# Performance work log

Measured on AMD Instinct MI355X. Metric: run time of the kernel, lower is better.

The kernel has to match this reference:

```python
import jax, jax.numpy as jnp
import numpy as np

D_MODEL = 1024
N_HEAD = 16
HEAD_DIM = D_MODEL // N_HEAD
D_FF = 4096
N_EXPERTS = 4
EPS = 1e-05


def _layer_norm(x, gamma, beta):
    mu = jnp.mean(x, axis=-1, keepdims=True)
    var = jnp.mean((x - mu) ** 2, axis=-1, keepdims=True)
    return (x - mu) / jnp.sqrt(var + EPS) * gamma + beta


def setup_inputs() -> dict:
    key = jax.random.key(0)
    ks = jax.random.split(key, 20)
    f32 = jnp.float32
    sc = 1.0 / np.sqrt(D_MODEL)
    scf = 1.0 / np.sqrt(D_FF)
    return {
        "src": jax.random.normal(ks[0], (4, 512, D_MODEL), f32),
        "Wq": jax.random.normal(ks[1], (D_MODEL, D_MODEL), f32) * sc,
        "bq": jnp.zeros((D_MODEL,), f32),
        "Wk": jax.random.normal(ks[2], (D_MODEL, D_MODEL), f32) * sc,
        "bk": jnp.zeros((D_MODEL,), f32),
        "Wv": jax.random.normal(ks[3], (D_MODEL, D_MODEL), f32) * sc,
        "bv": jnp.zeros((D_MODEL,), f32),
        "Wo": jax.random.normal(ks[4], (D_MODEL, D_MODEL), f32) * sc,
        "bo": jnp.zeros((D_MODEL,), f32),
        "router_w": jax.random.normal(ks[5], (D_MODEL, 1), f32) * 0.05,
        "router_b": jnp.zeros((1,), f32),
        "W1": jax.random.normal(ks[6], (N_EXPERTS, D_MODEL, D_FF), f32) * sc,
        "b1": jnp.zeros((N_EXPERTS, D_FF), f32),
        "W2": jax.random.normal(ks[7], (N_EXPERTS, D_FF, D_MODEL), f32) * scf,
        "b2": jnp.zeros((N_EXPERTS, D_MODEL), f32),
        "ln1_g": jnp.ones((D_MODEL,), f32),
        "ln1_b": jnp.zeros((D_MODEL,), f32),
        "ln2_g": jnp.ones((D_MODEL,), f32),
        "ln2_b": jnp.zeros((D_MODEL,), f32),
    }


def reference(src, Wq, bq, Wk, bk, Wv, bv, Wo, bo, router_w, router_b,
              W1, b1, W2, b2, ln1_g, ln1_b, ln2_g, ln2_b):
    B, T, _ = src.shape
    # --- self attention ---
    q = (src @ Wq + bq).reshape(B, T, N_HEAD, HEAD_DIM)
    k = (src @ Wk + bk).reshape(B, T, N_HEAD, HEAD_DIM)
    v = (src @ Wv + bv).reshape(B, T, N_HEAD, HEAD_DIM)
    scale = HEAD_DIM ** -0.5
    scores = jnp.einsum('bqhd,bkhd->bhqk', q, k) * scale
    probs = jax.nn.softmax(scores, axis=-1)
    attn = jnp.einsum('bhqk,bkhd->bqhd', probs, v).reshape(B, T, D_MODEL)
    attn = attn @ Wo + bo
    x = _layer_norm(src + attn, ln1_g, ln1_b)
    # --- hash-routed single-expert MoE FFN ---
    keys = (x @ router_w + router_b)[..., 0]           # [B, T]
    expert_idx = jnp.remainder(jnp.floor(keys).astype(jnp.int32), N_EXPERTS)
    ff_out = jnp.zeros_like(x)
    for e in range(N_EXPERTS):
        h = jax.nn.relu(x @ W1[e] + b1[e])             # [B, T, D_FF]
        y = h @ W2[e] + b2[e]                          # [B, T, D_MODEL]
        ff_out = ff_out + jnp.where((expert_idx == e)[..., None], y, 0.0)
    return _layer_norm(x + ff_out, ln2_g, ln2_b)
```

## Files before the change

### kernel.cpp

```cpp
#include <hip/hip_runtime.h>
#include <hip/hip_bf16.h>
#include <stdint.h>

typedef unsigned short u16;
typedef __attribute__((ext_vector_type(8))) short s8v;
typedef __attribute__((ext_vector_type(4))) float f4v;

#define DEVI static __device__ __forceinline__

DEVI u16 f2bf(float x) {
  union { float f; unsigned u; } a; a.f = x;
  return (u16)((a.u + 0x7fffu + ((a.u >> 16) & 1u)) >> 16);
}
DEVI float bf2f(u16 h) {
  union { float f; unsigned u; } a; a.u = ((unsigned)h) << 16; return a.f;
}
DEVI float wred_add(float s) {
#pragma unroll
  for (int o = 32; o; o >>= 1) s += __shfl_xor(s, o, 64);
  return s;
}
DEVI float wred_max(float s) {
#pragma unroll
  for (int o = 32; o; o >>= 1) s = fmaxf(s, __shfl_xor(s, o, 64));
  return s;
}
DEVI f4v mfma16(s8v a, s8v b, f4v c) {
  return __builtin_amdgcn_mfma_f32_16x16x32_bf16(a, b, c, 0, 0, 0);
}

DEVI void gload16(const u16* gp, u16* lp) {
  __builtin_amdgcn_global_load_lds(
      (const __attribute__((address_space(1))) uint32_t*)gp,
      (__attribute__((address_space(3))) uint32_t*)lp, 16, 0, 0);
}

DEVI s8v ldfrag_sw(const u16* base, int r, int lg) {
  const u16* row = base + r * 32;
  const int x = (r >> 1) & 3;
  const int hl = (lg & 1) * 4;
  const int g1 = lg >> 1;
  union { s8v v; uint2 u[2]; } t;
  t.u[0] = *(const uint2*)(row + ((g1 ^ x) * 8) + hl);
  t.u[1] = *(const uint2*)(row + (((g1 + 2) ^ x) * 8) + hl);
  return t.v;
}

__global__ __launch_bounds__(256) void split_k(const float* __restrict__ in,
                                               u16* __restrict__ h, u16* __restrict__ l, int n4) {
  int i = blockIdx.x * 256 + threadIdx.x;
  if (i >= n4) return;
  float4 v = ((const float4*)in)[i];
  ushort4 hv, lv;
  hv.x = f2bf(v.x); lv.x = f2bf(v.x - bf2f(hv.x));
  hv.y = f2bf(v.y); lv.y = f2bf(v.y - bf2f(hv.y));
  hv.z = f2bf(v.z); lv.z = f2bf(v.z - bf2f(hv.z));
  hv.w = f2bf(v.w); lv.w = f2bf(v.w - bf2f(hv.w));
  ((ushort4*)h)[i] = hv;
  ((ushort4*)l)[i] = lv;
}

template<bool LO>
__global__ __launch_bounds__(256) void transpose_split_k(const float* __restrict__ in, long long zIn,
                                                         u16* __restrict__ outH, u16* __restrict__ outL,
                                                         long long zOut, int R, int C) {
  __shared__ float t[32][33];
  in += (long long)blockIdx.z * zIn;
  outH += (long long)blockIdx.z * zOut;
  if (LO) outL += (long long)blockIdx.z * zOut;
  const int cc = blockIdx.x * 32, rr = blockIdx.y * 32;
  const int tx = threadIdx.x, ty = threadIdx.y;
#pragma unroll
  for (int i = 0; i < 4; ++i)
    t[ty * 4 + i][tx] = in[(long long)(rr + ty * 4 + i) * C + cc + tx];
  __syncthreads();
#pragma unroll
  for (int i = 0; i < 4; ++i) {
    float v = t[tx][ty * 4 + i];
    long long o = (long long)(cc + ty * 4 + i) * R + rr + tx;
    u16 h = f2bf(v);
    outH[o] = h;
    if (LO) outL[o] = f2bf(v - bf2f(h));
  }
}

__global__ __launch_bounds__(256) void transpose_pair_k(const u16* __restrict__ inH, const u16* __restrict__ inL,
                                                        u16* __restrict__ oH, u16* __restrict__ oL) {
  __shared__ u16 th[32][34], tl[32][34];
  const int b = blockIdx.z;
  const int dd = blockIdx.x * 32;
  const int tt = blockIdx.y * 32;
  const int tx = threadIdx.x, ty = threadIdx.y;
  const int64_t ibase = ((int64_t)(b * 512 + tt)) * 3072 + 2048 + dd;
#pragma unroll
  for (int i = 0; i < 4; ++i) {
    int rr = ty * 4 + i;
    th[rr][tx] = inH[ibase + (int64_t)rr * 3072 + tx];
    tl[rr][tx] = inL[ibase + (int64_t)rr * 3072 + tx];
  }
  __syncthreads();
  const int64_t obase = ((int64_t)b * 1024 + dd) * 512 + tt;
#pragma unroll
  for (int i = 0; i < 4; ++i) {
    int rr = ty * 4 + i;
    oH[obase + (int64_t)rr * 512 + tx] = th[tx][rr];
    oL[obase + (int64_t)rr * 512 + tx] = tl[tx][rr];
  }
}

__global__ __launch_bounds__(256) void catb_k(const float* __restrict__ a, const float* __restrict__ b,
                                              const float* __restrict__ c, float* __restrict__ o) {
  int i = blockIdx.x * 256 + threadIdx.x;
  if (i >= 3072) return;
  o[i] = i < 1024 ? a[i] : (i < 2048 ? b[i - 1024] : c[i - 2048]);
}

struct GemmArgs {
  const u16* Ah; const u16* Al; int lda;
  const u16* Bh; const u16* Bl; int ldb;
  float* C; u16* Ch; u16* Cl; int ldc;
  const float* bias;
  int K;
  int Z2;
  int64_t aZ1, aZ2, bZ1, bZ2, cZ1, cZ2;
  const int* ofs;
  int64_t bStrE; int biasStrE;
};

template<int BM, int BN, bool SPLIT, int EPI>
__global__ __launch_bounds__(256) void gemm_k(GemmArgs g) {
  constexpr int ASZ = BM * 32, BSZ = BN * 32;
  constexpr int AN = SPLIT ? 2 * ASZ : ASZ;
  constexpr int BNT = SPLIT ? 2 * BSZ : BSZ;
  __shared__ __align__(16) u16 sA[2][AN];
  __shared__ __align__(16) u16 sB[2][BNT];

  const int tid = threadIdx.x;
  const u16* Ah = g.Ah; const u16* Al = g.Al;
  const u16* Bh = g.Bh; const u16* Bl = g.Bl;
  int64_t cOff = 0;
  if (g.Z2 > 0) {
    int z1 = blockIdx.z / g.Z2, z2 = blockIdx.z % g.Z2;
    int64_t ao = (int64_t)z1 * g.aZ1 + (int64_t)z2 * g.aZ2;
    int64_t bo = (int64_t)z1 * g.bZ1 + (int64_t)z2 * g.bZ2;
    Ah += ao; Bh += bo;
    if (SPLIT) { Al += ao; Bl += bo; }
    cOff = (int64_t)z1 * g.cZ1 + (int64_t)z2 * g.cZ2;
  }
  const int row0 = blockIdx.x * BM;
  const int col0 = blockIdx.y * BN;
  const float* bias = g.bias;
  if (g.ofs) {
    if (row0 >= g.ofs[4]) return;
    int e = 0;
    while (e < 3 && row0 >= g.ofs[e + 1]) ++e;
    Bh += (int64_t)e * g.bStrE;
    if (bias) bias += (int64_t)e * g.biasStrE;
  }

  const int w = tid >> 6, lane = tid & 63;
  const int wr = w >> 1, wc = w & 1;
  const int lr = lane & 15, lg = lane >> 4;
  constexpr int FM = BM / 32, FN = BN / 32;

  const int srow = lane >> 2;
  const int sG = (lane & 3) ^ ((lane >> 3) & 3);

  auto stage = [&](int b, int kt) {
#pragma unroll
    for (int c = 0; c < BM / 64; ++c) {
      int ch = c * 4 + w;
      int64_t go = (int64_t)(row0 + ch * 16 + srow) * g.lda + kt + sG * 8;
      gload16(Ah + go, &sA[b][ch * 512]);
      if (SPLIT) gload16(Al + go, &sA[b][ASZ + ch * 512]);
    }
#pragma unroll
    for (int c = 0; c < BN / 64; ++c) {
      int ch = c * 4 + w;
      int64_t go = (int64_t)(col0 + ch * 16 + srow) * g.ldb + kt + sG * 8;
      gload16(Bh + go, &sB[b][ch * 512]);
      if (SPLIT) gload16(Bl + go, &sB[b][BSZ + ch * 512]);
    }
  };

  f4v acc[FM][FN];
#pragma unroll
  for (int i = 0; i < FM; ++i)
#pragma unroll
    for (int j = 0; j < FN; ++j) acc[i][j] = f4v{0.f, 0.f, 0.f, 0.f};

  stage(0, 0);
  __syncthreads();
  const int nt = g.K >> 5;
  for (int t = 0; t < nt; ++t) {
    const int cur = t & 1;
    if (t + 1 < nt) stage(cur ^ 1, (t + 1) << 5);
    s8v af[FM], bfr[FN], afl[SPLIT ? FM : 1], bfl[SPLIT ? FN : 1];
#pragma unroll
    for (int mi = 0; mi < FM; ++mi) {
      int r = wr * (BM / 2) + mi * 16 + lr;
      af[mi] = ldfrag_sw(&sA[cur][0], r, lg);
      if (SPLIT) afl[mi] = ldfrag_sw(&sA[cur][ASZ], r, lg);
    }
#pragma unroll
    for (int ni = 0; ni < FN; ++ni) {
      int r = wc * (BN / 2) + ni * 16 + lr;
      bfr[ni] = ldfrag_sw(&sB[cur][0], r, lg);
      if (SPLIT) bfl[ni] = ldfrag_sw(&sB[cur][BSZ], r, lg);
    }
#pragma unroll
    for (int mi = 0; mi < FM; ++mi)
#pragma unroll
      for (int ni = 0; ni < FN; ++ni) {
        acc[mi][ni] = mfma16(af[mi], bfr[ni], acc[mi][ni]);
        if (SPLIT) {
          acc[mi][ni] = mfma16(af[mi], bfl[ni], acc[mi][ni]);
          acc[mi][ni] = mfma16(afl[mi], bfr[ni], acc[mi][ni]);
        }
      }
    __syncthreads();
  }
#pragma unroll
  for (int mi = 0; mi < FM; ++mi) {
    int rbase = row0 + wr * (BM / 2) + mi * 16 + lg * 4;
#pragma unroll
    for (int ni = 0; ni < FN; ++ni) {
      int c = col0 + wc * (BN / 2) + ni * 16 + lr;
      float bv = bias ? bias[c] : 0.f;
#pragma unroll
      for (int j = 0; j < 4; ++j) {
        int r = rbase + j;
        float v = acc[mi][ni][j] + bv;
        if (EPI == 0) {
          g.C[cOff + (int64_t)r * g.ldc + c] = v;
        } else if (EPI == 1) {
          u16 h = f2bf(v);
          int64_t o = cOff + (int64_t)r * g.ldc + c;
          g.Ch[o] = h;
          g.Cl[o] = f2bf(v - bf2f(h));
        } else {
          v = v > 0.f ? v : 0.f;
          g.Ch[cOff + (int64_t)r * g.ldc + c] = f2bf(v);
        }
      }
    }
  }
}

__global__ __launch_bounds__(256) void reduce_k(const float* __restrict__ part, const int* __restrict__ rowsrc,
                                                const int* __restrict__ ofs, const float* __restrict__ b2,
                                                float* __restrict__ y) {
  int r = blockIdx.x;
  if (r >= ofs[4]) return;
  int s = rowsrc[r];
  if (s < 0) return;
  int e = 0;
  while (e < 3 && r >= ofs[e + 1]) ++e;
  int c = threadIdx.x;
  const int64_t RN = 2560ll * 1024;
  float4 v0 = ((const float4*)(part + 0 * RN + (int64_t)r * 1024))[c];
  float4 v1 = ((const float4*)(part + 1 * RN + (int64_t)r * 1024))[c];
  float4 v2 = ((const float4*)(part + 2 * RN + (int64_t)r * 1024))[c];
  float4 v3 = ((const float4*)(part + 3 * RN + (int64_t)r * 1024))[c];
  float4 bb = ((const float4*)(b2 + (int64_t)e * 1024))[c];
  float4 o;
  o.x = ((v0.x + v1.x) + v2.x) + v3.x + bb.x;
  o.y = ((v0.y + v1.y) + v2.y) + v3.y + bb.y;
  o.z = ((v0.z + v1.z) + v2.z) + v3.z + bb.z;
  o.w = ((v0.w + v1.w) + v2.w) + v3.w + bb.w;
  ((float4*)(y + (int64_t)s * 1024))[c] = o;
}

__global__ __launch_bounds__(128) void softmax_k(float* __restrict__ scores) {
  __shared__ float sm[2];
  const int64_t row = blockIdx.x;
  float* p = scores + row * 512;
  const int tid = threadIdx.x, w = tid >> 6, lane = tid & 63;
  float4 v = ((const float4*)p)[tid];
  v.x *= 0.125f; v.y *= 0.125f; v.z *= 0.125f; v.w *= 0.125f;
  float m = wred_max(fmaxf(fmaxf(v.x, v.y), fmaxf(v.z, v.w)));
  if (lane == 0) sm[w] = m;
  __syncthreads();
  m = fmaxf(sm[0], sm[1]);
  float e0 = expf(v.x - m), e1 = expf(v.y - m), e2 = expf(v.z - m), e3 = expf(v.w - m);
  float s = wred_add(e0 + e1 + e2 + e3);
  __syncthreads();
  if (lane == 0) sm[w] = s;
  __syncthreads();
  float inv = 1.f / (sm[0] + sm[1]);
  e0 *= inv; e1 *= inv; e2 *= inv; e3 *= inv;
  u16* ph = (u16*)p;
  ushort4 hv, lv;
  hv.x = f2bf(e0); lv.x = f2bf(e0 - bf2f(hv.x));
  hv.y = f2bf(e1); lv.y = f2bf(e1 - bf2f(hv.y));
  hv.z = f2bf(e2); lv.z = f2bf(e2 - bf2f(hv.z));
  hv.w = f2bf(e3); lv.w = f2bf(e3 - bf2f(hv.w));
  ((ushort4*)ph)[tid] = hv;
  ((ushort4*)(ph + 512))[tid] = lv;
}

__global__ __launch_bounds__(256) void ln_k(const float* __restrict__ a, const float* __restrict__ b,
                                            const float* __restrict__ gm, const float* __restrict__ bt,
                                            float* __restrict__ out) {
  __shared__ float sm[4];
  const int r = blockIdx.x, tid = threadIdx.x;
  const int w = tid >> 6, lane = tid & 63;
  float4 va = ((const float4*)(a + (int64_t)r * 1024))[tid];
  float4 vb = ((const float4*)(b + (int64_t)r * 1024))[tid];
  float x0 = va.x + vb.x, x1 = va.y + vb.y, x2 = va.z + vb.z, x3 = va.w + vb.w;
  float s = wred_add(x0 + x1 + x2 + x3);
  if (lane == 0) sm[w] = s;
  __syncthreads();
  float mu = (sm[0] + sm[1] + sm[2] + sm[3]) * (1.f / 1024.f);
  float d0 = x0 - mu, d1 = x1 - mu, d2 = x2 - mu, d3 = x3 - mu;
  float q = wred_add(d0 * d0 + d1 * d1 + d2 * d2 + d3 * d3);
  __syncthreads();
  if (lane == 0) sm[w] = q;
  __syncthreads();
  float var = (sm[0] + sm[1] + sm[2] + sm[3]) * (1.f / 1024.f);
  float rs = 1.f / sqrtf(var + 1e-5f);
  float4 g4 = ((const float4*)gm)[tid];
  float4 b4 = ((const float4*)bt)[tid];
  float4 o;
  o.x = d0 * rs * g4.x + b4.x;
  o.y = d1 * rs * g4.y + b4.y;
  o.z = d2 * rs * g4.z + b4.z;
  o.w = d3 * rs * g4.w + b4.w;
  ((float4*)(out + (int64_t)r * 1024))[tid] = o;
}

__global__ __launch_bounds__(256) void router_k(const float* __restrict__ x, const float* __restrict__ rw,
                                                const float* __restrict__ rb, int* __restrict__ eidx) {
  int t = blockIdx.x * 4 + (threadIdx.x >> 6);
  int lane = threadIdx.x & 63;
  const float* xr = x + (int64_t)t * 1024;
  float s = 0.f;
#pragma unroll
  for (int i = 0; i < 16; ++i) {
    int c = i * 64 + lane;
    s += xr[c] * rw[c];
  }
  s = wred_add(s);
  if (lane == 0) {
    float key = s + rb[0];
    int f = (int)floorf(key);
    eidx[t] = f & 3;
  }
}

__global__ __launch_bounds__(256) void compact_k(const int* __restrict__ eidx,
                                                 int* __restrict__ rowsrc, int* __restrict__ ofs) {
  __shared__ unsigned long long sc[256];
  __shared__ int soff[5];
  const int tid = threadIdx.x;
  int myE[8];
  unsigned long long c = 0;
#pragma unroll
  for (int i = 0; i < 8; ++i) {
    int e = eidx[tid * 8 + i];
    myE[i] = e;
    c += 1ull << (e * 16);
  }
  sc[tid] = c;
  __syncthreads();
  for (int o = 1; o < 256; o <<= 1) {
    unsigned long long v = (tid >= o) ? sc[tid - o] : 0ull;
    __syncthreads();
    sc[tid] += v;
    __syncthreads();
  }
  unsigned long long incl = sc[tid], tot = sc[255];
  unsigned long long excl = incl - c;
  if (tid == 0) {
    int off = 0;
    for (int e = 0; e < 4; ++e) {
      soff[e] = off;
      int cnt = (int)((tot >> (e * 16)) & 0xffff);
      off += (cnt + 127) & ~127;
    }
    soff[4] = off;
    for (int e = 0; e < 5; ++e) ofs[e] = soff[e];
  }
  __syncthreads();
  for (int r = tid; r < 2560; r += 256) rowsrc[r] = -1;
  __threadfence_block();
  __syncthreads();
  int rank[4];
#pragma unroll
  for (int e = 0; e < 4; ++e) rank[e] = (int)((excl >> (e * 16)) & 0xffff);
#pragma unroll
  for (int i = 0; i < 8; ++i) {
    int e = myE[i];
    rowsrc[soff[e] + rank[e]] = tid * 8 + i;
    rank[e]++;
  }
}

__global__ __launch_bounds__(256) void gather_k(const float* __restrict__ x, const int* __restrict__ rowsrc,
                                                const int* __restrict__ ofs, u16* __restrict__ xg) {
  int r = blockIdx.x;
  if (r >= ofs[4]) return;
  int s = rowsrc[r];
  int c = threadIdx.x;
  float4 v = (s >= 0) ? ((const float4*)(x + (int64_t)s * 1024))[c] : float4{0.f, 0.f, 0.f, 0.f};
  ushort4 o;
  o.x = f2bf(v.x); o.y = f2bf(v.y); o.z = f2bf(v.z); o.w = f2bf(v.w);
  ((ushort4*)(xg + (int64_t)r * 1024))[c] = o;
}

extern "C" void kernel_launch(void* const* d_in, const int* in_sizes, int n_in,
                              void* d_out, int out_size, void* d_ws, size_t ws_size,
                              hipStream_t stream) {
  const float* src = (const float*)d_in[0];
  const float* Wq  = (const float*)d_in[1];
  const float* bq  = (const float*)d_in[2];
  const float* Wk  = (const float*)d_in[3];
  const float* bk  = (const float*)d_in[4];
  const float* Wv  = (const float*)d_in[5];
  const float* bv  = (const float*)d_in[6];
  const float* Wo  = (const float*)d_in[7];
  const float* bo  = (const float*)d_in[8];
  const float* rw  = (const float*)d_in[9];
  const float* rb  = (const float*)d_in[10];
  const float* W1  = (const float*)d_in[11];
  const float* b1  = (const float*)d_in[12];
  const float* W2  = (const float*)d_in[13];
  const float* b2  = (const float*)d_in[14];
  const float* g1  = (const float*)d_in[15];
  const float* be1 = (const float*)d_in[16];
  const float* g2  = (const float*)d_in[17];
  const float* be2 = (const float*)d_in[18];
  float* out = (float*)d_out;

  char* base = (char*)d_ws;
  size_t off = 0;
  auto alloc = [&](size_t bytes) -> char* {
    char* p = base + off;
    off += (bytes + 255) & ~(size_t)255;
    return p;
  };
  const size_t MB = 1ull << 20;
  u16* srcH = (u16*)alloc(4 * MB);
  u16* srcL = (u16*)alloc(4 * MB);
  u16* WqkvTh = (u16*)alloc(6 * MB);
  u16* WqkvTl = (u16*)alloc(6 * MB);
  u16* WoTh = (u16*)alloc(2 * MB);
  u16* WoTl = (u16*)alloc(2 * MB);
  float* bqkv = (float*)alloc(16 * 1024);
  u16* qkvH = (u16*)alloc(12 * MB);
  u16* qkvL = (u16*)alloc(12 * MB);
  u16* hbuf = (u16*)qkvH;
  u16* vTH = (u16*)alloc(4 * MB); u16* vTL = (u16*)alloc(4 * MB);
  float* scores = (float*)alloc(64 * MB);
  u16* W1T = (u16*)scores;
  u16* W2T = (u16*)scores + 16ull * 1024 * 1024;
  u16* attnH = (u16*)alloc(4 * MB); u16* attnL = (u16*)alloc(4 * MB);
  u16* xg = (u16*)attnH;
  float* woOut = (float*)alloc(8 * MB);
  float* ybuf = (float*)woOut;
  float* xbuf = (float*)alloc(8 * MB);
  float* partials = (float*)alloc(40 * MB);
  int* eidx   = (int*)alloc(2048 * 4);
  int* rowsrc = (int*)alloc(2560 * 4);
  int* ofs    = (int*)alloc(32);
  (void)ws_size; (void)in_sizes; (void)n_in; (void)out_size;

  dim3 tb(32, 8);

  split_k<<<2048, 256, 0, stream>>>(src, srcH, srcL, 2048 * 1024 / 4);
  transpose_split_k<true><<<dim3(32, 32, 1), tb, 0, stream>>>(Wq, 0, WqkvTh, WqkvTl, 0, 1024, 1024);
  transpose_split_k<true><<<dim3(32, 32, 1), tb, 0, stream>>>(Wk, 0, WqkvTh + 1024 * 1024, WqkvTl + 1024 * 1024, 0, 1024, 1024);
  transpose_split_k<true><<<dim3(32, 32, 1), tb, 0, stream>>>(Wv, 0, WqkvTh + 2 * 1024 * 1024, WqkvTl + 2 * 1024 * 1024, 0, 1024, 1024);
  transpose_split_k<true><<<dim3(32, 32, 1), tb, 0, stream>>>(Wo, 0, WoTh, WoTl, 0, 1024, 1024);
  catb_k<<<12, 256, 0, stream>>>(bq, bk, bv, bqkv);

  {
    GemmArgs g{};
    g.Ah = srcH; g.Al = srcL; g.lda = 1024;
    g.Bh = WqkvTh; g.Bl = WqkvTl; g.ldb = 1024;
    g.Ch = qkvH; g.Cl = qkvL; g.ldc = 3072;
    g.bias = bqkv; g.K = 1024; g.Z2 = 0;
    gemm_k<128, 64, true, 1><<<dim3(16, 48, 1), 256, 0, stream>>>(g);
  }
  transpose_pair_k<<<dim3(32, 16, 4), tb, 0, stream>>>(qkvH, qkvL, vTH, vTL);

  {
    GemmArgs g{};
    g.Ah = qkvH; g.Al = qkvL; g.lda = 3072;
    g.Bh = qkvH + 1024; g.Bl = qkvL + 1024; g.ldb = 3072;
    g.C = scores; g.ldc = 512;
    g.K = 64; g.Z2 = 16;
    g.aZ1 = 512ll * 3072; g.aZ2 = 64;
    g.bZ1 = 512ll * 3072; g.bZ2 = 64;
    g.cZ1 = 16ll * 512 * 512; g.cZ2 = 512ll * 512;
    gemm_k<128, 64, true, 0><<<dim3(4, 8, 64), 256, 0, stream>>>(g);
  }
  softmax_k<<<64 * 512, 128, 0, stream>>>(scores);
  {
    GemmArgs g{};
    g.Ah = (const u16*)scores; g.Al = (const u16*)scores + 512; g.lda = 1024;
    g.Bh = vTH; g.Bl = vTL; g.ldb = 512;
    g.Ch = attnH; g.Cl = attnL; g.ldc = 1024;
    g.K = 512; g.Z2 = 16;
    g.aZ1 = 16ll * 512 * 1024; g.aZ2 = 512ll * 1024;
    g.bZ1 = 1024ll * 512;      g.bZ2 = 64ll * 512;
    g.cZ1 = 512ll * 1024;      g.cZ2 = 64;
    gemm_k<64, 64, true, 1><<<dim3(8, 1, 64), 256, 0, stream>>>(g);
  }
  {
    GemmArgs g{};
    g.Ah = attnH; g.Al = attnL; g.lda = 1024;
    g.Bh = WoTh; g.Bl = WoTl; g.ldb = 1024;
    g.C = woOut; g.ldc = 1024;
    g.bias = bo; g.K = 1024; g.Z2 = 0;
    gemm_k<64, 64, true, 0><<<dim3(32, 16, 1), 256, 0, stream>>>(g);
  }
  ln_k<<<2048, 256, 0, stream>>>(src, woOut, g1, be1, xbuf);

  router_k<<<512, 256, 0, stream>>>(xbuf, rw, rb, eidx);
  compact_k<<<1, 256, 0, stream>>>(eidx, rowsrc, ofs);
  gather_k<<<2560, 256, 0, stream>>>(xbuf, rowsrc, ofs, xg);

  transpose_split_k<false><<<dim3(128, 32, 4), tb, 0, stream>>>(W1, 1024ll * 4096, W1T, nullptr, 4096ll * 1024, 1024, 4096);
  transpose_split_k<false><<<dim3(32, 128, 4), tb, 0, stream>>>(W2, 4096ll * 1024, W2T, nullptr, 1024ll * 4096, 4096, 1024);

  {
    GemmArgs g{};
    g.Ah = xg; g.lda = 1024;
    g.Bh = W1T; g.ldb = 1024;
    g.Ch = hbuf; g.ldc = 4096;
    g.bias = b1; g.biasStrE = 4096;
    g.K = 1024; g.Z2 = 0;
    g.ofs = ofs; g.bStrE = 4096ll * 1024;
    gemm_k<128, 128, false, 2><<<dim3(20, 32, 1), 256, 0, stream>>>(g);
  }
  {
    GemmArgs g{};
    g.Ah = hbuf; g.lda = 4096;
    g.Bh = W2T; g.ldb = 4096;
    g.C = partials; g.ldc = 1024;
    g.bias = nullptr;
    g.K = 1024; g.Z2 = 4;
    g.aZ1 = 0; g.aZ2 = 1024;
    g.bZ1 = 0; g.bZ2 = 1024;
    g.cZ1 = 0; g.cZ2 = 2560ll * 1024;
    g.ofs = ofs; g.bStrE = 4096ll * 1024;
    gemm_k<128, 64, false, 0><<<dim3(20, 16, 4), 256, 0, stream>>>(g);
  }
  reduce_k<<<2560, 256, 0, stream>>>(partials, rowsrc, ofs, b2, ybuf);
  ln_k<<<2048, 256, 0, stream>>>(xbuf, ybuf, g2, be2, out);
}
```

Before: 335.8 us.

## Permute K within 32-blocks for single 128-bit LDS fragment reads and deepen prefetch

Producers of GEMM operands (split, transpose, gather, GEMM epilogues) now write the K dimension in a permuted order within each 32-element block. Each MFMA fragment can then be read from LDS with one 16-byte load instead of two 8-byte loads. The GEMM main loop also changes from single-buffer-ahead staging to issuing loads two tiles ahead, with explicit vmcnt/lgkmcnt waits and raw barriers. This cuts LDS instruction count and hides more global latency, but it couples the data layout across many kernels and risks subtle correctness errors if any producer and consumer disagree.

```diff
diff --git a/kernel.cpp b/kernel.cpp
--- a/kernel.cpp
+++ b/kernel.cpp
@@ -28,6 +28,8 @@
 DEVI f4v mfma16(s8v a, s8v b, f4v c) {
   return __builtin_amdgcn_mfma_f32_16x16x32_bf16(a, b, c, 0, 0, 0);
 }
+
+DEVI int rho(int j) { return ((j & 12) << 1) | (j & 3) | ((j >> 4) << 2); }
 
 DEVI void gload16(const u16* gp, u16* lp) {
   __builtin_amdgcn_global_load_lds(
@@ -36,14 +38,8 @@
 }
 
 DEVI s8v ldfrag_sw(const u16* base, int r, int lg) {
-  const u16* row = base + r * 32;
-  const int x = (r >> 1) & 3;
-  const int hl = (lg & 1) * 4;
-  const int g1 = lg >> 1;
-  union { s8v v; uint2 u[2]; } t;
-  t.u[0] = *(const uint2*)(row + ((g1 ^ x) * 8) + hl);
-  t.u[1] = *(const uint2*)(row + (((g1 + 2) ^ x) * 8) + hl);
-  return t.v;
+  int off = ((r >> 4) << 9) + ((r & 15) << 5) + ((lg ^ ((r >> 1) & 3)) << 3);
+  return *(const s8v*)(base + off);
 }
 
 __global__ __launch_bounds__(256) void split_k(const float* __restrict__ in,
@@ -56,8 +52,10 @@
   hv.y = f2bf(v.y); lv.y = f2bf(v.y - bf2f(hv.y));
   hv.z = f2bf(v.z); lv.z = f2bf(v.z - bf2f(hv.z));
   hv.w = f2bf(v.w); lv.w = f2bf(v.w - bf2f(hv.w));
-  ((ushort4*)h)[i] = hv;
-  ((ushort4*)l)[i] = lv;
+  int t = i & 7, blk = i >> 3;
+  int si = blk * 8 + ((t & 3) << 1) + (t >> 2);
+  ((ushort4*)h)[si] = hv;
+  ((ushort4*)l)[si] = lv;
 }
 
 template<bool LO>
@@ -74,10 +72,11 @@
   for (int i = 0; i < 4; ++i)
     t[ty * 4 + i][tx] = in[(long long)(rr + ty * 4 + i) * C + cc + tx];
   __syncthreads();
+  const int rtx = rho(tx);
 #pragma unroll
   for (int i = 0; i < 4; ++i) {
     float v = t[tx][ty * 4 + i];
-    long long o = (long long)(cc + ty * 4 + i) * R + rr + tx;
+    long long o = (long long)(cc + ty * 4 + i) * R + rr + rtx;
     u16 h = f2bf(v);
     outH[o] = h;
     if (LO) outL[o] = f2bf(v - bf2f(h));
@@ -92,19 +91,20 @@
   const int tt = blockIdx.y * 32;
   const int tx = threadIdx.x, ty = threadIdx.y;
   const int64_t ibase = ((int64_t)(b * 512 + tt)) * 3072 + 2048 + dd;
+  const int rtx = rho(tx);
 #pragma unroll
   for (int i = 0; i < 4; ++i) {
     int rr = ty * 4 + i;
-    th[rr][tx] = inH[ibase + (int64_t)rr * 3072 + tx];
-    tl[rr][tx] = inL[ibase + (int64_t)rr * 3072 + tx];
+    th[rr][tx] = inH[ibase + (int64_t)rr * 3072 + rtx];
+    tl[rr][tx] = inL[ibase + (int64_t)rr * 3072 + rtx];
   }
   __syncthreads();
   const int64_t obase = ((int64_t)b * 1024 + dd) * 512 + tt;
 #pragma unroll
   for (int i = 0; i < 4; ++i) {
     int rr = ty * 4 + i;
-    oH[obase + (int64_t)rr * 512 + tx] = th[tx][rr];
-    oL[obase + (int64_t)rr * 512 + tx] = tl[tx][rr];
+    oH[obase + (int64_t)rr * 512 + rtx] = th[tx][rr];
+    oL[obase + (int64_t)rr * 512 + rtx] = tl[tx][rr];
   }
 }
 
@@ -127,11 +127,12 @@
   int64_t bStrE; int biasStrE;
 };
 
-template<int BM, int BN, bool SPLIT, int EPI>
+template<int BM, int BN, bool SPLIT, int EPI, bool PN>
 __global__ __launch_bounds__(256) void gemm_k(GemmArgs g) {
   constexpr int ASZ = BM * 32, BSZ = BN * 32;
   constexpr int AN = SPLIT ? 2 * ASZ : ASZ;
   constexpr int BNT = SPLIT ? 2 * BSZ : BSZ;
+  constexpr int NLOAD = (BM / 64 + BN / 64) * (SPLIT ? 2 : 1);
   __shared__ __align__(16) u16 sA[2][AN];
   __shared__ __align__(16) u16 sB[2][BNT];
 
@@ -190,11 +191,14 @@
     for (int j = 0; j < FN; ++j) acc[i][j] = f4v{0.f, 0.f, 0.f, 0.f};
 
   stage(0, 0);
-  __syncthreads();
+  stage(1, 32);
+  asm volatile("s_waitcnt vmcnt(%0)" :: "n"(NLOAD) : "memory");
+  __builtin_amdgcn_sched_barrier(0);
+  __builtin_amdgcn_s_barrier();
+
   const int nt = g.K >> 5;
   for (int t = 0; t < nt; ++t) {
     const int cur = t & 1;
-    if (t + 1 < nt) stage(cur ^ 1, (t + 1) << 5);
     s8v af[FM], bfr[FN], afl[SPLIT ? FM : 1], bfl[SPLIT ? FN : 1];
 #pragma unroll
     for (int mi = 0; mi < FM; ++mi) {
@@ -208,6 +212,10 @@
       bfr[ni] = ldfrag_sw(&sB[cur][0], r, lg);
       if (SPLIT) bfl[ni] = ldfrag_sw(&sB[cur][BSZ], r, lg);
     }
+    asm volatile("s_waitcnt lgkmcnt(0)" ::: "memory");
+    __builtin_amdgcn_sched_barrier(0);
+    __builtin_amdgcn_s_barrier();
+    if (t + 2 < nt) stage(cur, (t + 2) << 5);
 #pragma unroll
     for (int mi = 0; mi < FM; ++mi)
 #pragma unroll
@@ -218,7 +226,14 @@
           acc[mi][ni] = mfma16(afl[mi], bfr[ni], acc[mi][ni]);
         }
       }
-    __syncthreads();
+    if (t + 1 < nt) {
+      if (t + 2 < nt)
+        asm volatile("s_waitcnt vmcnt(%0)" :: "n"(NLOAD) : "memory");
+      else
+        asm volatile("s_waitcnt vmcnt(0)" ::: "memory");
+      __builtin_amdgcn_sched_barrier(0);
+      __builtin_amdgcn_s_barrier();
+    }
   }
 #pragma unroll
   for (int mi = 0; mi < FM; ++mi) {
@@ -226,21 +241,26 @@
 #pragma unroll
     for (int ni = 0; ni < FN; ++ni) {
       int c = col0 + wc * (BN / 2) + ni * 16 + lr;
+      int cs = c;
+      if (PN) {
+        int jr = ((lr >> 2) << 3) | (lr & 3) | ((ni & 1) << 2);
+        cs = (c & ~31) | jr;
+      }
       float bv = bias ? bias[c] : 0.f;
 #pragma unroll
       for (int j = 0; j < 4; ++j) {
         int r = rbase + j;
         float v = acc[mi][ni][j] + bv;
         if (EPI == 0) {
-          g.C[cOff + (int64_t)r * g.ldc + c] = v;
+          g.C[cOff + (int64_t)r * g.ldc + cs] = v;
         } else if (EPI == 1) {
           u16 h = f2bf(v);
-          int64_t o = cOff + (int64_t)r * g.ldc + c;
+          int64_t o = cOff + (int64_t)r * g.ldc + cs;
           g.Ch[o] = h;
           g.Cl[o] = f2bf(v - bf2f(h));
         } else {
           v = v > 0.f ? v : 0.f;
-          g.Ch[cOff + (int64_t)r * g.ldc + c] = f2bf(v);
+          g.Ch[cOff + (int64_t)r * g.ldc + cs] = f2bf(v);
         }
       }
     }
@@ -405,7 +425,9 @@
   float4 v = (s >= 0) ? ((const float4*)(x + (int64_t)s * 1024))[c] : float4{0.f, 0.f, 0.f, 0.f};
   ushort4 o;
   o.x = f2bf(v.x); o.y = f2bf(v.y); o.z = f2bf(v.z); o.w = f2bf(v.w);
-  ((ushort4*)(xg + (int64_t)r * 1024))[c] = o;
+  int t = c & 7, blk = c >> 3;
+  int si = blk * 8 + ((t & 3) << 1) + (t >> 2);
+  ((ushort4*)(xg + (int64_t)r * 1024))[si] = o;
 }
 
 extern "C" void kernel_launch(void* const* d_in, const int* in_sizes, int n_in,
@@ -480,7 +502,7 @@
     g.Bh = WqkvTh; g.Bl = WqkvTl; g.ldb = 1024;
     g.Ch = qkvH; g.Cl = qkvL; g.ldc = 3072;
     g.bias = bqkv; g.K = 1024; g.Z2 = 0;
-    gemm_k<128, 64, true, 1><<<dim3(16, 48, 1), 256, 0, stream>>>(g);
+    gemm_k<128, 64, true, 1, true><<<dim3(16, 48, 1), 256, 0, stream>>>(g);
   }
   transpose_pair_k<<<dim3(32, 16, 4), tb, 0, stream>>>(qkvH, qkvL, vTH, vTL);
 
@@ -493,7 +515,7 @@
     g.aZ1 = 512ll * 3072; g.aZ2 = 64;
     g.bZ1 = 512ll * 3072; g.bZ2 = 64;
     g.cZ1 = 16ll * 512 * 512; g.cZ2 = 512ll * 512;
-    gemm_k<128, 64, true, 0><<<dim3(4, 8, 64), 256, 0, stream>>>(g);
+    gemm_k<128, 64, true, 0, true><<<dim3(4, 8, 64), 256, 0, stream>>>(g);
   }
   softmax_k<<<64 * 512, 128, 0, stream>>>(scores);
   {
@@ -505,7 +527,7 @@
     g.aZ1 = 16ll * 512 * 1024; g.aZ2 = 512ll * 1024;
     g.bZ1 = 1024ll * 512;      g.bZ2 = 64ll * 512;
     g.cZ1 = 512ll * 1024;      g.cZ2 = 64;
-    gemm_k<64, 64, true, 1><<<dim3(8, 1, 64), 256, 0, stream>>>(g);
+    gemm_k<64, 64, true, 1, true><<<dim3(8, 1, 64), 256, 0, stream>>>(g);
   }
   {
     GemmArgs g{};
@@ -513,7 +535,7 @@
     g.Bh = WoTh; g.Bl = WoTl; g.ldb = 1024;
     g.C = woOut; g.ldc = 1024;
     g.bias = bo; g.K = 1024; g.Z2 = 0;
-    gemm_k<64, 64, true, 0><<<dim3(32, 16, 1), 256, 0, stream>>>(g);
+    gemm_k<64, 64, true, 0, false><<<dim3(32, 16, 1), 256, 0, stream>>>(g);
   }
   ln_k<<<2048, 256, 0, stream>>>(src, woOut, g1, be1, xbuf);
 
@@ -532,7 +554,7 @@
     g.bias = b1; g.biasStrE = 4096;
     g.K = 1024; g.Z2 = 0;
     g.ofs = ofs; g.bStrE = 4096ll * 1024;
-    gemm_k<128, 128, false, 2><<<dim3(20, 32, 1), 256, 0, stream>>>(g);
+    gemm_k<128, 128, false, 2, true><<<dim3(20, 32, 1), 256, 0, stream>>>(g);
   }
   {
     GemmArgs g{};
@@ -545,7 +567,7 @@
     g.bZ1 = 0; g.bZ2 = 1024;
     g.cZ1 = 0; g.cZ2 = 2560ll * 1024;
     g.ofs = ofs; g.bStrE = 4096ll * 1024;
-    gemm_k<128, 64, false, 0><<<dim3(20, 16, 4), 256, 0, stream>>>(g);
+    gemm_k<128, 64, false, 0, false><<<dim3(20, 16, 4), 256, 0, stream>>>(g);
   }
   reduce_k<<<2560, 256, 0, stream>>>(partials, rowsrc, ofs, b2, ybuf);
   ln_k<<<2048, 256, 0, stream>>>(xbuf, ybuf, g2, be2, out);
```

Result: faster. 316.2 us (-5.8%).
